# Kernel optimization log

Measured on AMD Instinct MI355X. Metric: run time of the kernel, lower is better.

Reference implementation:

```python
import jax, jax.numpy as jnp
import numpy as np

N_NODES = 50000
N_EDGES = 800000
D_IN = 96
D_EDGE = 32
D_OUT = 96
N_TYPES = 4


def setup_inputs() -> dict:
    key = jax.random.key(0)
    k = jax.random.split(key, 6)
    x = jax.random.normal(k[0], (N_NODES, D_IN), dtype=jnp.float32)
    edge_features = jax.random.normal(k[1], (N_NODES, D_EDGE), dtype=jnp.float32)
    edge_index = jax.random.randint(k[2], (2, N_EDGES), 0, N_NODES, dtype=jnp.int32)
    edge_type = jax.random.randint(k[3], (N_EDGES,), 0, N_TYPES, dtype=jnp.int32)
    # One RelEdgeConv per relation type: Linear(D_IN + D_EDGE -> D_OUT) message fn
    scale = 1.0 / np.sqrt(D_IN + D_EDGE)
    W_msg = jax.random.uniform(k[4], (N_TYPES, D_IN + D_EDGE, D_OUT), jnp.float32, -scale, scale)
    b_msg = jax.random.uniform(k[5], (N_TYPES, D_OUT), jnp.float32, -scale, scale)
    return {"x": x, "edge_features": edge_features, "edge_index": edge_index,
            "edge_type": edge_type, "W_msg": W_msg, "b_msg": b_msg}


def reference(x, edge_features, edge_index, edge_type, W_msg, b_msg):
    # Node-level edge_features (shape[0] == N) -> per-edge relative features
    src, dst = edge_index[0], edge_index[1]
    e = jnp.abs(edge_features[src] - edge_features[dst])          # [E, De]
    feat = jnp.concatenate([x[src], e], axis=-1)                  # [E, Din+De]
    n_nodes = x.shape[0]
    n_types = W_msg.shape[0]

    def per_type(t):
        # relation mask: zero out messages for edges of other types
        mask = (edge_type == t).astype(x.dtype)[:, None]          # [E, 1]
        m = (feat @ W_msg[t] + b_msg[t]) * mask                   # [E, Dout]
        # scatter-add messages to destination nodes
        return jax.ops.segment_sum(m, dst, num_segments=n_nodes)  # [N, Dout]

    out = jnp.stack([per_type(t) for t in range(n_types)])        # [T, N, Dout]
    return out.mean(axis=0)
```

## Files before the change

kernel.cpp:

```cpp
#include <hip/hip_runtime.h>

#define E_EDGES 800000
#define NN 50000
#define D_IN 96
#define D_EDGE 32
#define D_OUT 96
#define KSUM 512
#define SSTRIDE 520
#define NB4 3125
#define ECAP 20
#define NKEYS 200000
#define NBINS 196
#define BINCAP 4608
#define SCATA 200
#define CHUNK 4000
#define CHIT 16
#define BUILD_BLOCKS 512

typedef __attribute__((ext_vector_type(8))) __bf16 bf16x8;
typedef __attribute__((ext_vector_type(4))) float floatx4;

__device__ __forceinline__ float lo16(unsigned int u) {
    return __builtin_bit_cast(float, u << 16);
}
__device__ __forceinline__ float hi16(unsigned int u) {
    return __builtin_bit_cast(float, u & 0xFFFF0000u);
}
__device__ __forceinline__ unsigned int pk2(float a, float b) {
    unsigned short ua = __builtin_bit_cast(unsigned short, (__bf16)a);
    unsigned short ub = __builtin_bit_cast(unsigned short, (__bf16)b);
    return (unsigned int)ua | ((unsigned int)ub << 16);
}

__global__ __launch_bounds__(256) void k_prep(const int* __restrict__ ei,
                                              const int* __restrict__ et,
                                              const float* __restrict__ x,
                                              const float* __restrict__ ef,
                                              const float* __restrict__ Wm,
                                              int* __restrict__ ccnt,
                                              int* __restrict__ CA,
                                              __bf16* __restrict__ WT,
                                              unsigned int* __restrict__ xeb) {
    __shared__ int h[NBINS], base[NBINS], c2[NBINS], gb[NBINS];
    __shared__ uint2 stage[CHUNK];
    int tid = threadIdx.x, bid = blockIdx.x;

    if (bid < SCATA) {
        int e0 = bid * CHUNK;
        for (int i = tid; i < NBINS; i += 256) h[i] = 0;
        __syncthreads();

        unsigned int rec[CHIT];
        int bn[CHIT];
#pragma unroll
        for (int it = 0; it < CHIT; it++) {
            int i = it * 256 + tid;
            bn[it] = -1;
            if (i < CHUNK) {
                int e = e0 + i;
                int dst = ei[E_EDGES + e];
                int ty  = et[e];
                int src = ei[e];
                rec[it] = ((unsigned)src << 10) | ((unsigned)(dst & 255) << 2)
                        | (unsigned)ty;
                int b = dst >> 8;
                bn[it] = b;
                atomicAdd(&h[b], 1);
            }
        }
        __syncthreads();

        if (tid < 64) {
            int lane = tid, carry = 0;
            for (int s = 0; s < NBINS; s += 64) {
                int idx = s + lane;
                int v = (idx < NBINS) ? h[idx] : 0;
                int sc = v;
                for (int d = 1; d < 64; d <<= 1) {
                    int t = __shfl_up(sc, d, 64);
                    if (lane >= d) sc += t;
                }
                if (idx < NBINS) { base[idx] = carry + sc - v; c2[idx] = carry + sc - v; }
                carry += __shfl(sc, 63, 64);
            }
        }
        __syncthreads();

#pragma unroll
        for (int it = 0; it < CHIT; it++) {
            if (bn[it] >= 0) {
                int pos = atomicAdd(&c2[bn[it]], 1);
                stage[pos] = make_uint2(rec[it], (unsigned)bn[it]);
            }
        }
        for (int b = tid; b < NBINS; b += 256)
            gb[b] = h[b] ? atomicAdd(&ccnt[b], h[b]) : 0;
        __syncthreads();

        for (int i = tid; i < CHUNK; i += 256) {
            uint2 s = stage[i];
            int b = (int)s.y;
            int pos = gb[b] + (i - base[b]);
            if (pos < BINCAP) CA[b * BINCAP + pos] = (int)s.x;
        }
    } else {
        int b2 = bid - SCATA;
        int gtid = b2 * 256 + tid;
        int lane = tid & 63, w = tid >> 6;
        for (int n = b2 * 4 + w; n < NN; n += BUILD_BLOCKS * 4) {
            float2 v;
            if (lane < 48) v = *(const float2*)(x  + (size_t)n * D_IN   + 2 * lane);
            else           v = *(const float2*)(ef + (size_t)n * D_EDGE + 2 * (lane - 48));
            xeb[(size_t)n * 64 + lane] = pk2(v.x, v.y);
        }
        for (int i = gtid; i < 96 * KSUM; i += BUILD_BLOCKS * 256) {
            int n = i >> 9, k = i & 511;
            WT[n * KSUM + k] = (__bf16)Wm[(size_t)k * 96 + n];
        }
    }
}

__global__ __launch_bounds__(256) void k_bin(const int* __restrict__ ccnt,
                                             const int* __restrict__ CA,
                                             int* __restrict__ cnt,
                                             int* __restrict__ eb) {
    __shared__ int kcnt[1024];
    int tid = threadIdx.x, c = blockIdx.x;
    for (int i = tid; i < 1024; i += 256) kcnt[i] = 0;
    __syncthreads();

    int m = min(ccnt[c], BINCAP);
    const int* src = CA + c * BINCAP;
    for (int i = tid; i < m; i += 256) {
        unsigned int r = (unsigned)src[i];
        int lk = (int)((r >> 2) & 255) * 4 + (int)(r & 3);
        int rk = atomicAdd(&kcnt[lk], 1);
        int key = c * 1024 + lk;
        if (rk < ECAP && key < NKEYS)
            eb[key * ECAP + rk] = (int)(r >> 10) << 6;
    }
    __syncthreads();
    for (int lk = tid; lk < 1024; lk += 256) {
        int key = c * 1024 + lk;
        if (key < NKEYS) cnt[key] = kcnt[lk];
    }
}

__global__ __launch_bounds__(256) void k_fused(const int* __restrict__ cursor,
                                               const int* __restrict__ eb,
                                               const unsigned int* __restrict__ xeb,
                                               const __bf16* __restrict__ WT,
                                               const float* __restrict__ bm,
                                               float* __restrict__ out) {
    __shared__ __align__(16) __bf16 Sl[16][SSTRIDE];
    __shared__ __align__(16) int el[64 * ECAP];
    __shared__ int h[64];

    int tid = threadIdx.x, lane = tid & 63, w = tid >> 6;
    int B = blockIdx.x;

    if (tid < 64) h[tid] = min(cursor[B * 64 + tid], ECAP);
    {
        const int4* s4 = (const int4*)(eb + (size_t)B * (64 * ECAP));
        int4* d4 = (int4*)el;
        for (int i = tid; i < (64 * ECAP) / 4; i += 256) d4[i] = s4[i];
    }
    __syncthreads();

    unsigned int Mmask = (lane >= 48) ? 0x7FFFFFFFu : 0xFFFFFFFFu;
    int quad = lane >> 4, low = lane & 15;

#define EDGE(u, k, nn, sa, sb) do {                                            \
        float f0 = lo16(u), f1 = hi16(u);                                      \
        f0 = __builtin_bit_cast(float,                                         \
                 __builtin_bit_cast(unsigned int, f0 - e0) & Mmask);           \
        f1 = __builtin_bit_cast(float,                                         \
                 __builtin_bit_cast(unsigned int, f1 - e1) & Mmask);           \
        sa += (i + k < nn) ? f0 : 0.f;                                         \
        sb += (i + k < nn) ? f1 : 0.f;                                         \
    } while (0)

    for (int j = 0; j < 4; j++) {
        int nl = w * 4 + j;
        int n = B * 16 + nl;
        float e0 = 0.f, e1 = 0.f;
        if (lane >= 48) {
            unsigned int u = xeb[(size_t)n * 64 + lane];
            e0 = lo16(u); e1 = hi16(u);
        }
        unsigned int* sp = (unsigned int*)&Sl[nl][0];

#pragma unroll
        for (int tp = 0; tp < 2; tp++) {
            int k0 = nl * 4 + 2 * tp;
            int n0 = h[k0], n1 = h[k0 + 1];
            const int* q0 = el + k0 * ECAP;
            const int* q1 = q0 + ECAP;
            float sa0 = 0.f, sb0 = 0.f, sa1 = 0.f, sb1 = 0.f;
            int mx = max(n0, n1);
            for (int i = 0; i < mx; i += 4) {
                unsigned int u0=0,u1=0,u2=0,u3=0, v0=0,v1=0,v2=0,v3=0;
                bool on0 = i < n0, on1 = i < n1;
                if (on0) {
                    int4 a = *(const int4*)(q0 + i);
                    int a1 = (i + 1 < n0) ? a.y : a.x;
                    int a2 = (i + 2 < n0) ? a.z : a.x;
                    int a3 = (i + 3 < n0) ? a.w : a.x;
                    u0 = xeb[a.x + lane]; u1 = xeb[a1 + lane];
                    u2 = xeb[a2 + lane]; u3 = xeb[a3 + lane];
                }
                if (on1) {
                    int4 b = *(const int4*)(q1 + i);
                    int b1 = (i + 1 < n1) ? b.y : b.x;
                    int b2 = (i + 2 < n1) ? b.z : b.x;
                    int b3 = (i + 3 < n1) ? b.w : b.x;
                    v0 = xeb[b.x + lane]; v1 = xeb[b1 + lane];
                    v2 = xeb[b2 + lane]; v3 = xeb[b3 + lane];
                }
                if (on0) { EDGE(u0,0,n0,sa0,sb0); EDGE(u1,1,n0,sa0,sb0);
                           EDGE(u2,2,n0,sa0,sb0); EDGE(u3,3,n0,sa0,sb0); }
                if (on1) { EDGE(v0,0,n1,sa1,sb1); EDGE(v1,1,n1,sa1,sb1);
                           EDGE(v2,2,n1,sa1,sb1); EDGE(v3,3,n1,sa1,sb1); }
            }
            sp[(2 * tp) * 64 + lane]     = pk2(sa0, sb0);
            sp[(2 * tp + 1) * 64 + lane] = pk2(sa1, sb1);
        }
    }
#undef EDGE
    __syncthreads();

    bf16x8 a[16];
    const __bf16* ap = &Sl[low][0] + quad * 8;
#pragma unroll
    for (int ks = 0; ks < 16; ks++) a[ks] = *(const bf16x8*)(ap + ks * 32);

    for (int ct = w; ct < 6; ct += 4) {
        floatx4 acc = {0.f, 0.f, 0.f, 0.f};
        const __bf16* bp = WT + (size_t)(ct * 16 + low) * KSUM + quad * 8;
#pragma unroll
        for (int ks = 0; ks < 16; ks++)
            acc = __builtin_amdgcn_mfma_f32_16x16x32_bf16(
                a[ks], *(const bf16x8*)(bp + ks * 32), acc, 0, 0, 0);
        int col = ct * 16 + low;
#pragma unroll
        for (int rg = 0; rg < 4; rg++) {
            int r = quad * 4 + rg;
            int g = B * 16 + r;
            float bias = (float)h[r * 4 + 0] * bm[col]
                       + (float)h[r * 4 + 1] * bm[96 + col]
                       + (float)h[r * 4 + 2] * bm[192 + col]
                       + (float)h[r * 4 + 3] * bm[288 + col];
            out[(size_t)g * D_OUT + col] = 0.25f * (acc[rg] + bias);
        }
    }
}

extern "C" void kernel_launch(void* const* d_in, const int* in_sizes, int n_in,
                              void* d_out, int out_size, void* d_ws, size_t ws_size,
                              hipStream_t stream) {
    const float* x  = (const float*)d_in[0];
    const float* ef = (const float*)d_in[1];
    const int*   ei = (const int*)d_in[2];
    const int*   et = (const int*)d_in[3];
    const float* Wm = (const float*)d_in[4];
    const float* bm = (const float*)d_in[5];
    float* out = (float*)d_out;

    int* ccnt = (int*)d_ws;
    int* cnt  = ccnt + 256;
    int* CA   = cnt + NKEYS;
    int* eb   = CA + NBINS * BINCAP;
    __bf16* WT  = (__bf16*)(eb + NKEYS * ECAP);
    unsigned int* xeb = (unsigned int*)(WT + 96 * KSUM);

    hipMemsetAsync(ccnt, 0, NBINS * sizeof(int), stream);
    k_prep <<<SCATA + BUILD_BLOCKS, 256, 0, stream>>>(ei, et, x, ef, Wm,
                                                      ccnt, CA, WT, xeb);
    k_bin  <<<NBINS, 256, 0, stream>>>(ccnt, CA, cnt, eb);
    k_fused<<<NB4, 256, 0, stream>>>(cnt, eb, xeb, WT, bm, out);
}
```

Baseline: 179.6 us.

## Pad edge lists to multiples of four and gather four relation lists per node together

The bucket builder now pads each per-key edge list up to a multiple of four with a self-pointer (the destination node's own row). The gather loop can then drop the per-edge bounds selects and process all four relation types of a node at once, giving more independent loads in flight. The padded entries contribute exactly zero to the edge-feature lanes, and their x contribution is subtracted with an fma correction. The scatter chunking constants also change. The cost is extra global writes for the padding and higher register pressure from sixteen outstanding gathers.

```diff
diff --git a/kernel.cpp b/kernel.cpp
--- a/kernel.cpp
+++ b/kernel.cpp
@@ -12,9 +12,9 @@
 #define NKEYS 200000
 #define NBINS 196
 #define BINCAP 4608
-#define SCATA 200
-#define CHUNK 4000
-#define CHIT 16
+#define SCATA 400
+#define CHUNK 2000
+#define CHIT 8
 #define BUILD_BLOCKS 512
 
 typedef __attribute__((ext_vector_type(8))) __bf16 bf16x8;
@@ -142,7 +142,14 @@
     __syncthreads();
     for (int lk = tid; lk < 1024; lk += 256) {
         int key = c * 1024 + lk;
-        if (key < NKEYS) cnt[key] = kcnt[lk];
+        if (key < NKEYS) {
+            int kc = kcnt[lk];
+            cnt[key] = kc;
+            int hh = min(kc, ECAP);
+            int pp = (hh + 3) & ~3;
+            int pv = (c * 256 + (lk >> 2)) << 6;
+            for (int rr = hh; rr < pp; rr++) eb[key * ECAP + rr] = pv;
+        }
     }
 }
 
@@ -170,61 +177,70 @@
     unsigned int Mmask = (lane >= 48) ? 0x7FFFFFFFu : 0xFFFFFFFFu;
     int quad = lane >> 4, low = lane & 15;
 
-#define EDGE(u, k, nn, sa, sb) do {                                            \
+#define EDGE(u, sa, sb) do {                                                   \
         float f0 = lo16(u), f1 = hi16(u);                                      \
         f0 = __builtin_bit_cast(float,                                         \
                  __builtin_bit_cast(unsigned int, f0 - e0) & Mmask);           \
         f1 = __builtin_bit_cast(float,                                         \
                  __builtin_bit_cast(unsigned int, f1 - e1) & Mmask);           \
-        sa += (i + k < nn) ? f0 : 0.f;                                         \
-        sb += (i + k < nn) ? f1 : 0.f;                                         \
+        sa += f0; sb += f1;                                                    \
     } while (0)
 
     for (int j = 0; j < 4; j++) {
         int nl = w * 4 + j;
         int n = B * 16 + nl;
-        float e0 = 0.f, e1 = 0.f;
-        if (lane >= 48) {
-            unsigned int u = xeb[(size_t)n * 64 + lane];
-            e0 = lo16(u); e1 = hi16(u);
-        }
+        unsigned int up = xeb[(size_t)n * 64 + lane];
+        float xd0 = lo16(up), xd1 = hi16(up);
+        float e0 = (lane >= 48) ? xd0 : 0.f;
+        float e1 = (lane >= 48) ? xd1 : 0.f;
+        float xc0 = (lane < 48) ? xd0 : 0.f;
+        float xc1 = (lane < 48) ? xd1 : 0.f;
         unsigned int* sp = (unsigned int*)&Sl[nl][0];
 
-#pragma unroll
-        for (int tp = 0; tp < 2; tp++) {
-            int k0 = nl * 4 + 2 * tp;
-            int n0 = h[k0], n1 = h[k0 + 1];
-            const int* q0 = el + k0 * ECAP;
-            const int* q1 = q0 + ECAP;
-            float sa0 = 0.f, sb0 = 0.f, sa1 = 0.f, sb1 = 0.f;
-            int mx = max(n0, n1);
-            for (int i = 0; i < mx; i += 4) {
-                unsigned int u0=0,u1=0,u2=0,u3=0, v0=0,v1=0,v2=0,v3=0;
-                bool on0 = i < n0, on1 = i < n1;
-                if (on0) {
-                    int4 a = *(const int4*)(q0 + i);
-                    int a1 = (i + 1 < n0) ? a.y : a.x;
-                    int a2 = (i + 2 < n0) ? a.z : a.x;
-                    int a3 = (i + 3 < n0) ? a.w : a.x;
-                    u0 = xeb[a.x + lane]; u1 = xeb[a1 + lane];
-                    u2 = xeb[a2 + lane]; u3 = xeb[a3 + lane];
-                }
-                if (on1) {
-                    int4 b = *(const int4*)(q1 + i);
-                    int b1 = (i + 1 < n1) ? b.y : b.x;
-                    int b2 = (i + 2 < n1) ? b.z : b.x;
-                    int b3 = (i + 3 < n1) ? b.w : b.x;
-                    v0 = xeb[b.x + lane]; v1 = xeb[b1 + lane];
-                    v2 = xeb[b2 + lane]; v3 = xeb[b3 + lane];
-                }
-                if (on0) { EDGE(u0,0,n0,sa0,sb0); EDGE(u1,1,n0,sa0,sb0);
-                           EDGE(u2,2,n0,sa0,sb0); EDGE(u3,3,n0,sa0,sb0); }
-                if (on1) { EDGE(v0,0,n1,sa1,sb1); EDGE(v1,1,n1,sa1,sb1);
-                           EDGE(v2,2,n1,sa1,sb1); EDGE(v3,3,n1,sa1,sb1); }
-            }
-            sp[(2 * tp) * 64 + lane]     = pk2(sa0, sb0);
-            sp[(2 * tp + 1) * 64 + lane] = pk2(sa1, sb1);
-        }
+        int h0 = h[nl * 4 + 0], h1 = h[nl * 4 + 1];
+        int h2 = h[nl * 4 + 2], h3 = h[nl * 4 + 3];
+        int p0 = (h0 + 3) & ~3, p1 = (h1 + 3) & ~3;
+        int p2 = (h2 + 3) & ~3, p3 = (h3 + 3) & ~3;
+        const int* q0 = el + (nl * 4 + 0) * ECAP;
+        const int* q1 = q0 + ECAP;
+        const int* q2 = q1 + ECAP;
+        const int* q3 = q2 + ECAP;
+        float sa0 = 0.f, sb0 = 0.f, sa1 = 0.f, sb1 = 0.f;
+        float sa2 = 0.f, sb2 = 0.f, sa3 = 0.f, sb3 = 0.f;
+        int mx = max(max(p0, p1), max(p2, p3));
+        for (int i = 0; i < mx; i += 4) {
+            bool o0 = i < p0, o1 = i < p1, o2 = i < p2, o3 = i < p3;
+            unsigned int ua0, ua1, ua2, ua3, ub0, ub1, ub2, ub3;
+            unsigned int uc0, uc1, uc2, uc3, ue0, ue1, ue2, ue3;
+            if (o0) { int4 a = *(const int4*)(q0 + i);
+                      ua0 = xeb[a.x + lane]; ua1 = xeb[a.y + lane];
+                      ua2 = xeb[a.z + lane]; ua3 = xeb[a.w + lane]; }
+            if (o1) { int4 a = *(const int4*)(q1 + i);
+                      ub0 = xeb[a.x + lane]; ub1 = xeb[a.y + lane];
+                      ub2 = xeb[a.z + lane]; ub3 = xeb[a.w + lane]; }
+            if (o2) { int4 a = *(const int4*)(q2 + i);
+                      uc0 = xeb[a.x + lane]; uc1 = xeb[a.y + lane];
+                      uc2 = xeb[a.z + lane]; uc3 = xeb[a.w + lane]; }
+            if (o3) { int4 a = *(const int4*)(q3 + i);
+                      ue0 = xeb[a.x + lane]; ue1 = xeb[a.y + lane];
+                      ue2 = xeb[a.z + lane]; ue3 = xeb[a.w + lane]; }
+            if (o0) { EDGE(ua0, sa0, sb0); EDGE(ua1, sa0, sb0);
+                      EDGE(ua2, sa0, sb0); EDGE(ua3, sa0, sb0); }
+            if (o1) { EDGE(ub0, sa1, sb1); EDGE(ub1, sa1, sb1);
+                      EDGE(ub2, sa1, sb1); EDGE(ub3, sa1, sb1); }
+            if (o2) { EDGE(uc0, sa2, sb2); EDGE(uc1, sa2, sb2);
+                      EDGE(uc2, sa2, sb2); EDGE(uc3, sa2, sb2); }
+            if (o3) { EDGE(ue0, sa3, sb3); EDGE(ue1, sa3, sb3);
+                      EDGE(ue2, sa3, sb3); EDGE(ue3, sa3, sb3); }
+        }
+        sa0 = fmaf((float)(h0 - p0), xc0, sa0); sb0 = fmaf((float)(h0 - p0), xc1, sb0);
+        sa1 = fmaf((float)(h1 - p1), xc0, sa1); sb1 = fmaf((float)(h1 - p1), xc1, sb1);
+        sa2 = fmaf((float)(h2 - p2), xc0, sa2); sb2 = fmaf((float)(h2 - p2), xc1, sb2);
+        sa3 = fmaf((float)(h3 - p3), xc0, sa3); sb3 = fmaf((float)(h3 - p3), xc1, sb3);
+        sp[0 * 64 + lane] = pk2(sa0, sb0);
+        sp[1 * 64 + lane] = pk2(sa1, sb1);
+        sp[2 * 64 + lane] = pk2(sa2, sb2);
+        sp[3 * 64 + lane] = pk2(sa3, sb3);
     }
 #undef EDGE
     __syncthreads();
```

Measured after the change: 179.5 us. Within noise of the previous version (-0.1%).
